# Performance work log

Measured on AMD Instinct MI355X. Metric: run time of the kernel, lower is better.

Reference implementation:

```python
import jax, jax.numpy as jnp
import numpy as np

E, D, H, T = 8, 1024, 2048, 2048  # num_expert, d_model, d_hidden, tokens

def setup_inputs() -> dict:
    key = jax.random.key(0)
    ks = jax.random.split(key, 7)
    return {
        "moe_inp": jax.random.normal(ks[0], (T, D), jnp.float32),
        "Wg": jax.random.normal(ks[1], (D, E), jnp.float32) * 0.02,
        "bg": jnp.zeros((E,), jnp.float32),
        "W1": jax.random.normal(ks[2], (E, D, H), jnp.float32) * 0.02,
        "b1": jnp.zeros((E, H), jnp.float32),
        "W2": jax.random.normal(ks[3], (E, H, D), jnp.float32) * 0.02,
        "b2": jnp.zeros((E, D), jnp.float32),
        "top_k": 2,
    }

def reference(moe_inp, Wg, bg, W1, b1, W2, b2, top_k):
    # NaiveGate: linear gate, top-k select, softmax over the selected logits
    logits = moe_inp @ Wg + bg                      # [T, E]
    top_vals, top_idx = jax.lax.top_k(logits, top_k)  # [T, k]
    gate_score = jax.nn.softmax(top_vals, axis=-1)    # [T, k]

    # Exact (no capacity drop) MoE: scan over experts, mask-combine.
    # Equivalent math to scatter -> per-expert FFN -> gather -> bmm(gate_score, ...).
    def body(acc, xs):
        e, w1, bb1, w2, bb2 = xs
        h = jax.nn.gelu(moe_inp @ w1 + bb1)          # [T, H]
        y = h @ w2 + bb2                             # [T, D]
        w = jnp.sum(jnp.where(top_idx == e, gate_score, 0.0), axis=-1)  # [T]
        return acc + w[:, None] * y, None

    init = jnp.zeros_like(moe_inp)
    xs = (jnp.arange(E), W1, b1, W2, b2)
    moe_outp, _ = jax.lax.scan(body, init, xs)
    return moe_outp, top_idx
```

## Files before the change

### kernel.cpp

```cpp
#include <hip/hip_runtime.h>
#include <stdint.h>

#define T_TOK 2048
#define D_DIM 1024
#define H_DIM 2048
#define N_EXP 8
#define MAXS  5120

#define WS_CNT    0
#define WS_POFF   64
#define WS_BTOK   256
#define WS_BW     (WS_BTOK + N_EXP*2048*4)
#define WS_XG     (WS_BW + N_EXP*2048*4)
#define WS_HBUF   (WS_XG + (size_t)MAXS*1024*2)
#define WS_W1T    (WS_HBUF + (size_t)MAXS*2048*2)
#define WS_W2T    (WS_W1T + (size_t)N_EXP*1024*2048*2)

typedef __bf16 bf16x8 __attribute__((ext_vector_type(8)));
typedef float  f32x4  __attribute__((ext_vector_type(4)));

__device__ __forceinline__ unsigned short f2bf(float f) {
  unsigned int u = __float_as_uint(f);
  u += 0x7fffu + ((u >> 16) & 1u);
  return (unsigned short)(u >> 16);
}

__device__ __forceinline__ float gelu_tanh(float x) {
  float u = 0.7978845608028654f * (x + 0.044715f * x * x * x);
  return 0.5f * x * (1.0f + tanhf(u));
}

__global__ void zero_kernel(float4* __restrict__ out4, int* __restrict__ cnt) {
  int i = blockIdx.x * 256 + threadIdx.x;
  out4[i] = make_float4(0.f, 0.f, 0.f, 0.f);
  if (blockIdx.x == 0 && threadIdx.x < N_EXP) cnt[threadIdx.x] = 0;
}

__global__ void gate_kernel(const float* __restrict__ x, const float* __restrict__ Wg,
                            const float* __restrict__ bg, float* __restrict__ out_idx,
                            int* __restrict__ cnt, int* __restrict__ btok,
                            float* __restrict__ bw) {
  const int lane = threadIdx.x & 63;
  const int t = blockIdx.x * 4 + (threadIdx.x >> 6);
  float p[8];
#pragma unroll
  for (int i = 0; i < 8; ++i) p[i] = 0.f;
  const float* xr = x + (size_t)t * D_DIM;
  for (int i = lane; i < D_DIM; i += 64) {
    const float xv = xr[i];
    const float4 wa = ((const float4*)(Wg + i * 8))[0];
    const float4 wb = ((const float4*)(Wg + i * 8))[1];
    p[0] += xv * wa.x; p[1] += xv * wa.y; p[2] += xv * wa.z; p[3] += xv * wa.w;
    p[4] += xv * wb.x; p[5] += xv * wb.y; p[6] += xv * wb.z; p[7] += xv * wb.w;
  }
#pragma unroll
  for (int off = 32; off > 0; off >>= 1) {
#pragma unroll
    for (int i = 0; i < 8; ++i) p[i] += __shfl_xor(p[i], off);
  }
  if (lane == 0) {
#pragma unroll
    for (int i = 0; i < 8; ++i) p[i] += bg[i];
    int i0 = 0; float v0 = p[0];
#pragma unroll
    for (int i = 1; i < 8; ++i) if (p[i] > v0) { v0 = p[i]; i0 = i; }
    int i1 = -1; float v1 = -3.4e38f;
#pragma unroll
    for (int i = 0; i < 8; ++i) if (i != i0 && p[i] > v1) { v1 = p[i]; i1 = i; }
    const float ex = expf(v1 - v0);
    const float inv = 1.f / (1.f + ex);
    out_idx[t * 2 + 0] = (float)i0;
    out_idx[t * 2 + 1] = (float)i1;
    int s0 = atomicAdd(&cnt[i0], 1);
    btok[i0 * 2048 + s0] = t; bw[i0 * 2048 + s0] = inv;
    int s1 = atomicAdd(&cnt[i1], 1);
    btok[i1 * 2048 + s1] = t; bw[i1 * 2048 + s1] = ex * inv;
  }
}

__global__ void header_kernel(const int* __restrict__ cnt, int* __restrict__ poff) {
  if (threadIdx.x == 0) {
    int off = 0;
    for (int e = 0; e < N_EXP; ++e) { poff[e] = off; off += ((cnt[e] + 127) >> 7) << 7; }
    poff[N_EXP] = off;
  }
}

__global__ void transpose_cvt(const float* __restrict__ W1, unsigned short* __restrict__ W1t,
                              const float* __restrict__ W2, unsigned short* __restrict__ W2t) {
  const int set = blockIdx.z;
  const int e = blockIdx.y;
  const int lin = blockIdx.x;
  const int R = set ? H_DIM : D_DIM;
  const int C = set ? D_DIM : H_DIM;
  const int tx = set ? (lin & 15) : (lin & 31);
  const int ty = set ? (lin >> 4) : (lin >> 5);
  const float* in = (set ? W2 : W1) + (size_t)e * (D_DIM * H_DIM);
  unsigned short* out = (set ? W2t : W1t) + (size_t)e * (D_DIM * H_DIM);
  const int c0 = tx * 64, r0 = ty * 64;
  __shared__ float tile[64][68];
  const int tid = threadIdx.x;
#pragma unroll
  for (int p = 0; p < 4; ++p) {
    const int idx = p * 256 + tid;
    const int r = idx >> 4, c4 = idx & 15;
    *(float4*)&tile[r][c4 * 4] = *(const float4*)(in + (size_t)(r0 + r) * C + c0 + c4 * 4);
  }
  __syncthreads();
#pragma unroll
  for (int p = 0; p < 2; ++p) {
    const int idx = p * 256 + tid;
    const int oc = idx >> 3, seg = idx & 7;
    unsigned u[4];
#pragma unroll
    for (int j = 0; j < 4; ++j) {
      const unsigned lo = f2bf(tile[seg * 8 + 2 * j][oc]);
      const unsigned hi = f2bf(tile[seg * 8 + 2 * j + 1][oc]);
      u[j] = lo | (hi << 16);
    }
    *(uint4*)(out + (size_t)(c0 + oc) * R + r0 + seg * 8) = make_uint4(u[0], u[1], u[2], u[3]);
  }
}

__global__ void gather_cvt(const float* __restrict__ x, const int* __restrict__ poff,
                           const int* __restrict__ cnt, const int* __restrict__ btok,
                           unsigned short* __restrict__ Xg) {
  const int s = blockIdx.x;
  if (s >= poff[N_EXP]) return;
  int e = 0;
#pragma unroll
  for (int i = 0; i < N_EXP; ++i) if (s >= poff[i + 1]) e = i + 1;
  const int local = s - poff[e];
  uint2* orow = (uint2*)(Xg + (size_t)s * D_DIM);
  if (local < cnt[e]) {
    const int t = btok[e * 2048 + local];
    const float4 v = ((const float4*)(x + (size_t)t * D_DIM))[threadIdx.x];
    uint2 u;
    u.x = (unsigned)f2bf(v.x) | ((unsigned)f2bf(v.y) << 16);
    u.y = (unsigned)f2bf(v.z) | ((unsigned)f2bf(v.w) << 16);
    orow[threadIdx.x] = u;
  } else {
    orow[threadIdx.x] = make_uint2(0u, 0u);
  }
}

template <int MODE>
__global__ void __launch_bounds__(256) moe_gemm(
    const unsigned short* __restrict__ A, const unsigned short* __restrict__ B,
    const float* __restrict__ bias, const int* __restrict__ poff,
    const int* __restrict__ cnt, const int* __restrict__ btok,
    const float* __restrict__ bw, unsigned short* __restrict__ Hout,
    float* __restrict__ out) {
  constexpr int K   = (MODE == 0) ? D_DIM : H_DIM;
  constexpr int NT  = (MODE == 0) ? H_DIM / 128 : D_DIM / 128;
  constexpr int SK  = (MODE == 0) ? 1 : 2;
  constexpr int KS  = K / SK;
  constexpr int NIT = KS / 32;

  const int lin  = blockIdx.x;
  const int glo  = lin & 7;
  const int mt   = (lin >> 3) & 15;
  const int g    = ((lin >> 7) << 3) | glo;
  const int nt   = g % NT;
  const int rest = g / NT;
  const int e    = rest & 7;
  const int ksl  = rest >> 3;

  const int base = poff[e];
  const int pcnt = poff[e + 1] - base;
  if (mt * 128 >= pcnt) return;
  const int row0 = base + mt * 128;
  const int n0 = nt * 128;

  __shared__ __align__(16) unsigned short As[2][128 * 32];
  __shared__ __align__(16) unsigned short Bs[2][128 * 32];

  const int tid = threadIdx.x;
  const int lane = tid & 63;
  const int wv = tid >> 6;
  const int wm = wv >> 1;
  const int wn = wv & 1;

  const unsigned short* Ab = A + (size_t)row0 * K + ksl * KS;
  const unsigned short* Bb = B + (size_t)e * ((size_t)H_DIM * D_DIM) + (size_t)n0 * K + ksl * KS;

  f32x4 acc[4][4];
#pragma unroll
  for (int i = 0; i < 4; ++i)
#pragma unroll
    for (int j = 0; j < 4; ++j) acc[i][j] = (f32x4)(0.0f);

  const int subr = lane >> 2;
  const int ks = (lane & 3) * 8;
  const int fr = lane & 15;
  const int kq = (lane >> 4) * 8;

  auto stage = [&](int kt, int b) {
    const int k0 = kt * 32;
#pragma unroll
    for (int it = 0; it < 2; ++it) {
      const int ci = wv + it * 4;
      const int r = ci * 16 + subr;
      const unsigned short* ga = Ab + (size_t)r * K + (k0 + ks);
      const unsigned short* gb = Bb + (size_t)r * K + (k0 + ks);
      __builtin_amdgcn_global_load_lds(
          (__attribute__((address_space(1))) void*)ga,
          (__attribute__((address_space(3))) void*)(As[b] + ci * 16 * 32), 16, 0, 0);
      __builtin_amdgcn_global_load_lds(
          (__attribute__((address_space(1))) void*)gb,
          (__attribute__((address_space(3))) void*)(Bs[b] + ci * 16 * 32), 16, 0, 0);
    }
  };

  stage(0, 0);
  for (int i = 0; i < NIT; ++i) {
    const int b = i & 1;
    __syncthreads();
    if (i + 1 < NIT) stage(i + 1, b ^ 1);
    bf16x8 av[4], bv[4];
#pragma unroll
    for (int mi = 0; mi < 4; ++mi)
      av[mi] = *(const bf16x8*)(As[b] + (wm * 64 + mi * 16 + fr) * 32 + kq);
#pragma unroll
    for (int ni = 0; ni < 4; ++ni)
      bv[ni] = *(const bf16x8*)(Bs[b] + (wn * 64 + ni * 16 + fr) * 32 + kq);
#pragma unroll
    for (int mi = 0; mi < 4; ++mi)
#pragma unroll
      for (int ni = 0; ni < 4; ++ni)
        acc[mi][ni] = __builtin_amdgcn_mfma_f32_16x16x32_bf16(av[mi], bv[ni], acc[mi][ni], 0, 0, 0);
  }

  if (MODE == 0) {
    const float* bb = bias + (size_t)e * H_DIM + n0;
#pragma unroll
    for (int mi = 0; mi < 4; ++mi) {
      const int rb = wm * 64 + mi * 16 + (lane >> 4) * 4;
#pragma unroll
      for (int r = 0; r < 4; ++r) {
        unsigned short* hp = Hout + (size_t)(row0 + rb + r) * H_DIM + n0;
#pragma unroll
        for (int ni = 0; ni < 4; ++ni) {
          const int col = wn * 64 + ni * 16 + fr;
          hp[col] = f2bf(gelu_tanh(acc[mi][ni][r] + bb[col]));
        }
      }
    }
  } else {
    const float* bb = bias + (size_t)e * D_DIM + n0;
    const int ce = cnt[e];
#pragma unroll
    for (int mi = 0; mi < 4; ++mi) {
      const int rb = wm * 64 + mi * 16 + (lane >> 4) * 4;
#pragma unroll
      for (int r = 0; r < 4; ++r) {
        const int local = mt * 128 + rb + r;
        if (local < ce) {
          const int tok = btok[e * 2048 + local];
          const float w = bw[e * 2048 + local];
          float* op = out + (size_t)tok * D_DIM + n0;
#pragma unroll
          for (int ni = 0; ni < 4; ++ni) {
            const int col = wn * 64 + ni * 16 + fr;
            const float bias_once = (ksl == 0) ? bb[col] : 0.f;
            atomicAdd(op + col, w * (acc[mi][ni][r] + bias_once));
          }
        }
      }
    }
  }
}

extern "C" void kernel_launch(void* const* d_in, const int* in_sizes, int n_in,
                              void* d_out, int out_size, void* d_ws, size_t ws_size,
                              hipStream_t stream) {
  const float* moe_inp = (const float*)d_in[0];
  const float* Wg = (const float*)d_in[1];
  const float* bg = (const float*)d_in[2];
  const float* W1 = (const float*)d_in[3];
  const float* b1 = (const float*)d_in[4];
  const float* W2 = (const float*)d_in[5];
  const float* b2 = (const float*)d_in[6];
  float* out = (float*)d_out;

  char* ws = (char*)d_ws;
  int* cnt  = (int*)(ws + WS_CNT);
  int* poff = (int*)(ws + WS_POFF);
  int* btok = (int*)(ws + WS_BTOK);
  float* bw = (float*)(ws + WS_BW);
  unsigned short* Xg   = (unsigned short*)(ws + WS_XG);
  unsigned short* Hbuf = (unsigned short*)(ws + WS_HBUF);
  unsigned short* W1t  = (unsigned short*)(ws + WS_W1T);
  unsigned short* W2t  = (unsigned short*)(ws + WS_W2T);

  zero_kernel<<<dim3(2048), dim3(256), 0, stream>>>((float4*)out, cnt);
  gate_kernel<<<dim3(T_TOK / 4), dim3(256), 0, stream>>>(moe_inp, Wg, bg,
                                                         out + (size_t)T_TOK * D_DIM,
                                                         cnt, btok, bw);
  header_kernel<<<dim3(1), dim3(64), 0, stream>>>(cnt, poff);
  transpose_cvt<<<dim3(512, N_EXP, 2), dim3(256), 0, stream>>>(W1, W1t, W2, W2t);
  gather_cvt<<<dim3(MAXS), dim3(256), 0, stream>>>(moe_inp, poff, cnt, btok, Xg);
  moe_gemm<0><<<dim3(2048), dim3(256), 0, stream>>>(
      Xg, W1t, b1, poff, cnt, btok, bw, Hbuf, nullptr);
  moe_gemm<1><<<dim3(2048), dim3(256), 0, stream>>>(
      Hbuf, W2t, b2, poff, cnt, btok, bw, nullptr, out);
}
```

Measured before the change: 348.8 us.

## Shrink MoE GEMM M-tile to 64 and compute expert offsets inline

Expert segments are now padded to 64 rows instead of 128, and the grouped GEMMs use 64x128 tiles with twice as many blocks, which cuts wasted padding rows and raises block count. The separate header kernel is removed, and each block recomputes prefix offsets from the counts. In exchange each tile has lower arithmetic intensity, since B tiles are reloaded for more M-tiles and each wave holds fewer accumulators.

```diff
diff --git a/kernel.cpp b/kernel.cpp
--- a/kernel.cpp
+++ b/kernel.cpp
@@ -5,10 +5,9 @@
 #define D_DIM 1024
 #define H_DIM 2048
 #define N_EXP 8
-#define MAXS  5120
+#define MAXS  4608
 
 #define WS_CNT    0
-#define WS_POFF   64
 #define WS_BTOK   256
 #define WS_BW     (WS_BTOK + N_EXP*2048*4)
 #define WS_XG     (WS_BW + N_EXP*2048*4)
@@ -75,14 +74,6 @@
     btok[i0 * 2048 + s0] = t; bw[i0 * 2048 + s0] = inv;
     int s1 = atomicAdd(&cnt[i1], 1);
     btok[i1 * 2048 + s1] = t; bw[i1 * 2048 + s1] = ex * inv;
-  }
-}
-
-__global__ void header_kernel(const int* __restrict__ cnt, int* __restrict__ poff) {
-  if (threadIdx.x == 0) {
-    int off = 0;
-    for (int e = 0; e < N_EXP; ++e) { poff[e] = off; off += ((cnt[e] + 127) >> 7) << 7; }
-    poff[N_EXP] = off;
   }
 }
 
@@ -122,18 +113,34 @@
   }
 }
 
-__global__ void gather_cvt(const float* __restrict__ x, const int* __restrict__ poff,
-                           const int* __restrict__ cnt, const int* __restrict__ btok,
-                           unsigned short* __restrict__ Xg) {
+__device__ __forceinline__ void expert_seg(const int* __restrict__ cnt, int e,
+                                           int& base, int& ce, int& pcnt, int& total) {
+  int off = 0; base = 0; ce = 0; pcnt = 0;
+#pragma unroll
+  for (int i = 0; i < N_EXP; ++i) {
+    const int c = cnt[i];
+    const int p = (c + 63) & ~63;
+    if (i == e) { base = off; ce = c; pcnt = p; }
+    off += p;
+  }
+  total = off;
+}
+
+__global__ void gather_cvt(const float* __restrict__ x, const int* __restrict__ cnt,
+                           const int* __restrict__ btok, unsigned short* __restrict__ Xg) {
   const int s = blockIdx.x;
-  if (s >= poff[N_EXP]) return;
-  int e = 0;
-#pragma unroll
-  for (int i = 0; i < N_EXP; ++i) if (s >= poff[i + 1]) e = i + 1;
-  const int local = s - poff[e];
+  int off = 0, e = -1, loc = 0, c_e = 0;
+#pragma unroll
+  for (int i = 0; i < N_EXP; ++i) {
+    const int c = cnt[i];
+    const int p = (c + 63) & ~63;
+    if (e < 0 && s < off + p) { e = i; loc = s - off; c_e = c; }
+    off += p;
+  }
+  if (e < 0) return;
   uint2* orow = (uint2*)(Xg + (size_t)s * D_DIM);
-  if (local < cnt[e]) {
-    const int t = btok[e * 2048 + local];
+  if (loc < c_e) {
+    const int t = btok[e * 2048 + loc];
     const float4 v = ((const float4*)(x + (size_t)t * D_DIM))[threadIdx.x];
     uint2 u;
     u.x = (unsigned)f2bf(v.x) | ((unsigned)f2bf(v.y) << 16);
@@ -147,32 +154,29 @@
 template <int MODE>
 __global__ void __launch_bounds__(256) moe_gemm(
     const unsigned short* __restrict__ A, const unsigned short* __restrict__ B,
-    const float* __restrict__ bias, const int* __restrict__ poff,
-    const int* __restrict__ cnt, const int* __restrict__ btok,
-    const float* __restrict__ bw, unsigned short* __restrict__ Hout,
-    float* __restrict__ out) {
+    const float* __restrict__ bias, const int* __restrict__ cnt,
+    const int* __restrict__ btok, const float* __restrict__ bw,
+    unsigned short* __restrict__ Hout, float* __restrict__ out) {
   constexpr int K   = (MODE == 0) ? D_DIM : H_DIM;
-  constexpr int NT  = (MODE == 0) ? H_DIM / 128 : D_DIM / 128;
   constexpr int SK  = (MODE == 0) ? 1 : 2;
   constexpr int KS  = K / SK;
   constexpr int NIT = KS / 32;
 
-  const int lin  = blockIdx.x;
-  const int glo  = lin & 7;
-  const int mt   = (lin >> 3) & 15;
-  const int g    = ((lin >> 7) << 3) | glo;
-  const int nt   = g % NT;
-  const int rest = g / NT;
-  const int e    = rest & 7;
-  const int ksl  = rest >> 3;
-
-  const int base = poff[e];
-  const int pcnt = poff[e + 1] - base;
-  if (mt * 128 >= pcnt) return;
-  const int row0 = base + mt * 128;
+  const int lin = blockIdx.x;
+  const int glo = lin & 7;
+  const int mt  = (lin >> 3) & 31;
+  const int g   = ((lin >> 8) << 3) | glo;
+  int nt, e, ksl;
+  if (MODE == 0) { nt = g & 15; e = g >> 4; ksl = 0; }
+  else           { nt = g & 7;  e = (g >> 3) & 7; ksl = g >> 6; }
+
+  int base, ce, pcnt, total;
+  expert_seg(cnt, e, base, ce, pcnt, total);
+  if (mt * 64 >= pcnt) return;
+  const int row0 = base + mt * 64;
   const int n0 = nt * 128;
 
-  __shared__ __align__(16) unsigned short As[2][128 * 32];
+  __shared__ __align__(16) unsigned short As[2][64 * 32];
   __shared__ __align__(16) unsigned short Bs[2][128 * 32];
 
   const int tid = threadIdx.x;
@@ -184,9 +188,9 @@
   const unsigned short* Ab = A + (size_t)row0 * K + ksl * KS;
   const unsigned short* Bb = B + (size_t)e * ((size_t)H_DIM * D_DIM) + (size_t)n0 * K + ksl * KS;
 
-  f32x4 acc[4][4];
-#pragma unroll
-  for (int i = 0; i < 4; ++i)
+  f32x4 acc[2][4];
+#pragma unroll
+  for (int i = 0; i < 2; ++i)
 #pragma unroll
     for (int j = 0; j < 4; ++j) acc[i][j] = (f32x4)(0.0f);
 
@@ -197,15 +201,18 @@
 
   auto stage = [&](int kt, int b) {
     const int k0 = kt * 32;
+    {
+      const int r = wv * 16 + subr;
+      const unsigned short* ga = Ab + (size_t)r * K + (k0 + ks);
+      __builtin_amdgcn_global_load_lds(
+          (__attribute__((address_space(1))) void*)ga,
+          (__attribute__((address_space(3))) void*)(As[b] + wv * 16 * 32), 16, 0, 0);
+    }
 #pragma unroll
     for (int it = 0; it < 2; ++it) {
       const int ci = wv + it * 4;
       const int r = ci * 16 + subr;
-      const unsigned short* ga = Ab + (size_t)r * K + (k0 + ks);
       const unsigned short* gb = Bb + (size_t)r * K + (k0 + ks);
-      __builtin_amdgcn_global_load_lds(
-          (__attribute__((address_space(1))) void*)ga,
-          (__attribute__((address_space(3))) void*)(As[b] + ci * 16 * 32), 16, 0, 0);
       __builtin_amdgcn_global_load_lds(
           (__attribute__((address_space(1))) void*)gb,
           (__attribute__((address_space(3))) void*)(Bs[b] + ci * 16 * 32), 16, 0, 0);
@@ -217,15 +224,15 @@
     const int b = i & 1;
     __syncthreads();
     if (i + 1 < NIT) stage(i + 1, b ^ 1);
-    bf16x8 av[4], bv[4];
-#pragma unroll
-    for (int mi = 0; mi < 4; ++mi)
-      av[mi] = *(const bf16x8*)(As[b] + (wm * 64 + mi * 16 + fr) * 32 + kq);
+    bf16x8 av[2], bv[4];
+#pragma unroll
+    for (int mi = 0; mi < 2; ++mi)
+      av[mi] = *(const bf16x8*)(As[b] + (wm * 32 + mi * 16 + fr) * 32 + kq);
 #pragma unroll
     for (int ni = 0; ni < 4; ++ni)
       bv[ni] = *(const bf16x8*)(Bs[b] + (wn * 64 + ni * 16 + fr) * 32 + kq);
 #pragma unroll
-    for (int mi = 0; mi < 4; ++mi)
+    for (int mi = 0; mi < 2; ++mi)
 #pragma unroll
       for (int ni = 0; ni < 4; ++ni)
         acc[mi][ni] = __builtin_amdgcn_mfma_f32_16x16x32_bf16(av[mi], bv[ni], acc[mi][ni], 0, 0, 0);
@@ -234,8 +241,8 @@
   if (MODE == 0) {
     const float* bb = bias + (size_t)e * H_DIM + n0;
 #pragma unroll
-    for (int mi = 0; mi < 4; ++mi) {
-      const int rb = wm * 64 + mi * 16 + (lane >> 4) * 4;
+    for (int mi = 0; mi < 2; ++mi) {
+      const int rb = wm * 32 + mi * 16 + (lane >> 4) * 4;
 #pragma unroll
       for (int r = 0; r < 4; ++r) {
         unsigned short* hp = Hout + (size_t)(row0 + rb + r) * H_DIM + n0;
@@ -248,13 +255,12 @@
     }
   } else {
     const float* bb = bias + (size_t)e * D_DIM + n0;
-    const int ce = cnt[e];
-#pragma unroll
-    for (int mi = 0; mi < 4; ++mi) {
-      const int rb = wm * 64 + mi * 16 + (lane >> 4) * 4;
+#pragma unroll
+    for (int mi = 0; mi < 2; ++mi) {
+      const int rb = wm * 32 + mi * 16 + (lane >> 4) * 4;
 #pragma unroll
       for (int r = 0; r < 4; ++r) {
-        const int local = mt * 128 + rb + r;
+        const int local = mt * 64 + rb + r;
         if (local < ce) {
           const int tok = btok[e * 2048 + local];
           const float w = bw[e * 2048 + local];
@@ -285,7 +291,6 @@
 
   char* ws = (char*)d_ws;
   int* cnt  = (int*)(ws + WS_CNT);
-  int* poff = (int*)(ws + WS_POFF);
   int* btok = (int*)(ws + WS_BTOK);
   float* bw = (float*)(ws + WS_BW);
   unsigned short* Xg   = (unsigned short*)(ws + WS_XG);
@@ -297,11 +302,10 @@
   gate_kernel<<<dim3(T_TOK / 4), dim3(256), 0, stream>>>(moe_inp, Wg, bg,
                                                          out + (size_t)T_TOK * D_DIM,
                                                          cnt, btok, bw);
-  header_kernel<<<dim3(1), dim3(64), 0, stream>>>(cnt, poff);
   transpose_cvt<<<dim3(512, N_EXP, 2), dim3(256), 0, stream>>>(W1, W1t, W2, W2t);
-  gather_cvt<<<dim3(MAXS), dim3(256), 0, stream>>>(moe_inp, poff, cnt, btok, Xg);
-  moe_gemm<0><<<dim3(2048), dim3(256), 0, stream>>>(
-      Xg, W1t, b1, poff, cnt, btok, bw, Hbuf, nullptr);
-  moe_gemm<1><<<dim3(2048), dim3(256), 0, stream>>>(
-      Hbuf, W2t, b2, poff, cnt, btok, bw, nullptr, out);
-}
+  gather_cvt<<<dim3(MAXS), dim3(256), 0, stream>>>(moe_inp, cnt, btok, Xg);
+  moe_gemm<0><<<dim3(4096), dim3(256), 0, stream>>>(
+      Xg, W1t, b1, cnt, btok, bw, Hbuf, nullptr);
+  moe_gemm<1><<<dim3(4096), dim3(256), 0, stream>>>(
+      Hbuf, W2t, b2, cnt, btok, bw, nullptr, out);
+}
```

Result: faster. 339.8 us (-2.6%).
